# Optimization experiments

Hardware: AMD Instinct MI355X
Metric: run time of the kernel (lower is better)

The kernel has to match this reference:

```python
import jax, jax.numpy as jnp
import numpy as np

B, T, C = 4, 2048, 1024
NH = 16
HD = C // NH


def setup_inputs() -> dict:
    key = jax.random.key(0)
    ks = jax.random.split(key, 5)
    s = 1.0 / np.sqrt(C)
    return {
        "x": jax.random.normal(ks[0], (B, T, C), dtype=jnp.float32),
        "W_qkv": jax.random.normal(ks[1], (C, 3 * C), dtype=jnp.float32) * s,
        "b_qkv": jnp.zeros((3 * C,), dtype=jnp.float32),
        "W_out": jax.random.normal(ks[2], (C, C), dtype=jnp.float32) * s,
        "b_out": jnp.zeros((C,), dtype=jnp.float32),
    }


def reference(x, W_qkv, b_qkv, W_out, b_out):
    Bx, Tx, Cx = x.shape
    qkv = x @ W_qkv + b_qkv                      # [B,T,3C]
    q, k, v = jnp.split(qkv, 3, axis=2)
    # [B,T,C] -> [B,NH,T,HD]
    q = q.reshape(Bx, Tx, NH, HD).transpose(0, 2, 1, 3)
    k = k.reshape(Bx, Tx, NH, HD).transpose(0, 2, 1, 3)
    v = v.reshape(Bx, Tx, NH, HD).transpose(0, 2, 1, 3)
    scale = 1.0 / np.sqrt(HD).astype(np.float32)
    attn = jnp.einsum('bhqd,bhkd->bhqk', q, k) * scale  # [B,NH,T,T]
    causal = jnp.tril(jnp.ones((Tx, Tx), dtype=bool))
    attn = jnp.where(causal[None, None], attn, jnp.float32(-jnp.inf))
    attn = jax.nn.softmax(attn, axis=-1)
    out = jnp.einsum('bhqk,bhkd->bhqd', attn, v)        # [B,NH,T,HD]
    out = out.transpose(0, 2, 1, 3).reshape(Bx, Tx, Cx)
    y = out @ W_out + b_out
    return (y, k, v)
```

## Files before the change

kernel.cpp:

```cpp
#include <hip/hip_runtime.h>
#include <cstdint>
#include <cstddef>

typedef __bf16 bf16x8 __attribute__((ext_vector_type(8)));
typedef __bf16 bf16x4 __attribute__((ext_vector_type(4)));
typedef float  f32x4  __attribute__((ext_vector_type(4)));

#define MFMA16(a, b, c) __builtin_amdgcn_mfma_f32_16x16x32_bf16((a), (b), (c), 0, 0, 0)

#define GLL16(gsrc, ldst)                                                              \
  __builtin_amdgcn_global_load_lds((__attribute__((address_space(1))) void*)(gsrc),    \
                                   (__attribute__((address_space(3))) void*)(ldst),    \
                                   16, 0, 0)

#define QSCALE 0.1803368801111204f


__global__ __launch_bounds__(256)
void cvt_f32_bf16(const float* __restrict__ in, __bf16* __restrict__ out, int n4)
{
    int i = blockIdx.x * 256 + threadIdx.x;
    if (i < n4) {
        float4 v = ((const float4*)in)[i];
        bf16x4 o;
        o[0] = (__bf16)v.x; o[1] = (__bf16)v.y; o[2] = (__bf16)v.z; o[3] = (__bf16)v.w;
        ((bf16x4*)out)[i] = o;
    }
}

__global__ __launch_bounds__(256)
void transpose_cvt(const float* __restrict__ in, __bf16* __restrict__ out, int K, int N)
{
    __shared__ __bf16 tile[32][33];
    const int n0 = blockIdx.x * 32, k0 = blockIdx.y * 32;
    const int tx = threadIdx.x, ty = threadIdx.y;
    #pragma unroll
    for (int i = 0; i < 4; ++i)
        tile[ty + i * 8][tx] = (__bf16)in[(size_t)(k0 + ty + i * 8) * N + n0 + tx];
    __syncthreads();
    #pragma unroll
    for (int i = 0; i < 4; ++i)
        out[(size_t)(n0 + ty + i * 8) * K + k0 + tx] = tile[tx][ty + i * 8];
}


__global__ __launch_bounds__(256)
void vtrans(const float* __restrict__ vout, __bf16* __restrict__ vwst)
{
    const int bh = blockIdx.y;
    const int t0 = blockIdx.x * 64;
    const int tid = threadIdx.x;

    __shared__ __bf16 VT[64][68];

    const int tr = tid >> 4;
    const int dc = (tid & 15) * 4;

    float4 vals[4];
    #pragma unroll
    for (int i = 0; i < 4; ++i)
        vals[i] = *(const float4*)&vout[((size_t)bh * 2048 + t0 + tr + 16 * i) * 64 + dc];

    #pragma unroll
    for (int j = 0; j < 4; ++j) {
        bf16x4 pk;
        pk[0] = (__bf16)(&vals[0].x)[j];
        pk[1] = (__bf16)(&vals[1].x)[j];
        pk[2] = (__bf16)(&vals[2].x)[j];
        pk[3] = (__bf16)(&vals[3].x)[j];
        *(bf16x4*)&VT[dc + j][4 * tr] = pk;
    }
    __syncthreads();

    #pragma unroll
    for (int k = 0; k < 2; ++k) {
        const int c = tid + 256 * k;
        const int d = c >> 3, off = (c & 7) * 8;
        bf16x8 v = *(const bf16x8*)&VT[d][off];
        *(bf16x8*)&vwst[((size_t)bh * 64 + d) * 2048 + t0 + off] = v;
    }
}


__global__ __launch_bounds__(256)
void gemm_qkv(const __bf16* __restrict__ A, const __bf16* __restrict__ Bt,
              const float* __restrict__ bias,
              __bf16* __restrict__ qws, float* __restrict__ kout, float* __restrict__ vout,
              __bf16* __restrict__ kws)
{
    constexpr int K = 1024;
    const int d   = blockIdx.y * 24 + blockIdx.x;
    const int xcd = d & 7, loc = d >> 3;
    const int m0 = (xcd * 8 + (loc & 7)) * 128;
    const int n0 = (loc >> 3) * 128;
    const int tid = threadIdx.x;
    const int wave = tid >> 6, lane = tid & 63;
    const int quad = lane >> 4, lr = lane & 15;
    const int wrow = (wave & 1) * 64, wcol = (wave >> 1) * 64;

    __shared__ __bf16 As[128 * 32];
    __shared__ __bf16 Bs[128 * 32];

    f32x4 acc[4][4];
    #pragma unroll
    for (int mi = 0; mi < 4; ++mi)
      #pragma unroll
      for (int ni = 0; ni < 4; ++ni)
        #pragma unroll
        for (int c = 0; c < 4; ++c) acc[mi][ni][c] = 0.f;

    const int u0 = tid, u1 = tid + 256;
    const int cg0 = ((u0 & 3) ^ ((u0 >> 3) & 3)) * 8;
    const int cg1 = ((u1 & 3) ^ ((u1 >> 3) & 3)) * 8;
    const __bf16* ga0 = A  + (size_t)(m0 + (u0 >> 2)) * K + cg0;
    const __bf16* ga1 = A  + (size_t)(m0 + (u1 >> 2)) * K + cg1;
    const __bf16* gb0 = Bt + (size_t)(n0 + (u0 >> 2)) * K + cg0;
    const __bf16* gb1 = Bt + (size_t)(n0 + (u1 >> 2)) * K + cg1;
    __bf16* la0 = As + u0 * 8;
    __bf16* la1 = As + u1 * 8;
    __bf16* lb0 = Bs + u0 * 8;
    __bf16* lb1 = Bs + u1 * 8;

    const int sw = (quad ^ ((lr >> 1) & 3)) * 8;

    for (int kt = 0; kt < K; kt += 32) {
        __syncthreads();
        GLL16(ga0 + kt, la0);
        GLL16(ga1 + kt, la1);
        GLL16(gb0 + kt, lb0);
        GLL16(gb1 + kt, lb1);
        __syncthreads();
        bf16x8 af[4], bfv[4];
        #pragma unroll
        for (int mi = 0; mi < 4; ++mi)
            af[mi] = *(const bf16x8*)&As[(wrow + mi * 16 + lr) * 32 + sw];
        #pragma unroll
        for (int ni = 0; ni < 4; ++ni)
            bfv[ni] = *(const bf16x8*)&Bs[(wcol + ni * 16 + lr) * 32 + sw];
        #pragma unroll
        for (int mi = 0; mi < 4; ++mi)
          #pragma unroll
          for (int ni = 0; ni < 4; ++ni)
            acc[mi][ni] = MFMA16(af[mi], bfv[ni], acc[mi][ni]);
    }

    const int sec = n0 >> 10;
    #pragma unroll
    for (int ni = 0; ni < 4; ++ni) {
        const int gn = n0 + wcol + ni * 16 + lr;
        const float bv = bias[gn];
        const int cn = gn & 1023, hh = cn >> 6, dd = cn & 63;
        #pragma unroll
        for (int mi = 0; mi < 4; ++mi) {
            const int gm0 = m0 + wrow + mi * 16 + quad * 4;
            const int b = gm0 >> 11, t0 = gm0 & 2047;
            const size_t tb = ((size_t)b * 16 + hh) * 2048;
            if (sec == 0) {
                #pragma unroll
                for (int r = 0; r < 4; ++r)
                    qws[(tb + t0 + r) * 64 + dd] = (__bf16)((acc[mi][ni][r] + bv) * QSCALE);
            } else if (sec == 1) {
                #pragma unroll
                for (int r = 0; r < 4; ++r) {
                    const float val = acc[mi][ni][r] + bv;
                    kout[(tb + t0 + r) * 64 + dd] = val;
                    kws [(tb + t0 + r) * 64 + dd] = (__bf16)val;
                }
            } else {
                #pragma unroll
                for (int r = 0; r < 4; ++r)
                    vout[(tb + t0 + r) * 64 + dd] = acc[mi][ni][r] + bv;
            }
        }
    }
}


__global__ __launch_bounds__(256)
void gemm_out(const __bf16* __restrict__ A, const __bf16* __restrict__ Bt,
              const float* __restrict__ bias, float* __restrict__ y)
{
    constexpr int K = 1024;
    const int m0 = blockIdx.y * 64, n0 = blockIdx.x * 128;
    const int tid = threadIdx.x;
    const int wave = tid >> 6, lane = tid & 63;
    const int quad = lane >> 4, lr = lane & 15;
    const int wrow = (wave & 1) * 32, wcol = (wave >> 1) * 64;

    __shared__ __bf16 As[64 * 32];
    __shared__ __bf16 Bs[128 * 32];

    f32x4 acc[2][4];
    #pragma unroll
    for (int mi = 0; mi < 2; ++mi)
      #pragma unroll
      for (int ni = 0; ni < 4; ++ni)
        #pragma unroll
        for (int c = 0; c < 4; ++c) acc[mi][ni][c] = 0.f;

    const int ua = tid, u0 = tid, u1 = tid + 256;
    const int cga = ((ua & 3) ^ ((ua >> 3) & 3)) * 8;
    const int cg0 = ((u0 & 3) ^ ((u0 >> 3) & 3)) * 8;
    const int cg1 = ((u1 & 3) ^ ((u1 >> 3) & 3)) * 8;
    const __bf16* ga  = A  + (size_t)(m0 + (ua >> 2)) * K + cga;
    const __bf16* gb0 = Bt + (size_t)(n0 + (u0 >> 2)) * K + cg0;
    const __bf16* gb1 = Bt + (size_t)(n0 + (u1 >> 2)) * K + cg1;
    __bf16* la  = As + ua * 8;
    __bf16* lb0 = Bs + u0 * 8;
    __bf16* lb1 = Bs + u1 * 8;

    const int sw = (quad ^ ((lr >> 1) & 3)) * 8;

    for (int kt = 0; kt < K; kt += 32) {
        __syncthreads();
        GLL16(ga + kt, la);
        GLL16(gb0 + kt, lb0);
        GLL16(gb1 + kt, lb1);
        __syncthreads();
        bf16x8 af[2], bfv[4];
        #pragma unroll
        for (int mi = 0; mi < 2; ++mi)
            af[mi] = *(const bf16x8*)&As[(wrow + mi * 16 + lr) * 32 + sw];
        #pragma unroll
        for (int ni = 0; ni < 4; ++ni)
            bfv[ni] = *(const bf16x8*)&Bs[(wcol + ni * 16 + lr) * 32 + sw];
        #pragma unroll
        for (int mi = 0; mi < 2; ++mi)
          #pragma unroll
          for (int ni = 0; ni < 4; ++ni)
            acc[mi][ni] = MFMA16(af[mi], bfv[ni], acc[mi][ni]);
    }

    #pragma unroll
    for (int ni = 0; ni < 4; ++ni) {
        const int gn = n0 + wcol + ni * 16 + lr;
        const float bv = bias[gn];
        #pragma unroll
        for (int mi = 0; mi < 2; ++mi) {
            #pragma unroll
            for (int r = 0; r < 4; ++r) {
                const int gm = m0 + wrow + mi * 16 + quad * 4 + r;
                y[(size_t)gm * 1024 + gn] = acc[mi][ni][r] + bv;
            }
        }
    }
}


__global__ __launch_bounds__(256, 2)
void attn_fused(const __bf16* __restrict__ qws, const __bf16* __restrict__ kws,
                const __bf16* __restrict__ vwst, __bf16* __restrict__ attnws)
{
    const int bh = blockIdx.x;
    const int tid = threadIdx.x;
    const int wave = tid >> 6, lane = tid & 63;
    const int quad = lane >> 4, lr = lane & 15;

    const int jqp[2] = { (int)blockIdx.y, 15 - (int)blockIdx.y };
    const int ntp[2] = { 2 * (jqp[0] + 1), 2 * (jqp[1] + 1) };
    const int nt0 = ntp[0];
    const int ntot = 34;

    __shared__ __bf16 Ks [3][2][64][32];
    __shared__ __bf16 Vts[3][2][64][32];
    __shared__ __bf16 Ps [4][32][72];

    const int srow = tid >> 2;
    const int scg  = ((tid & 3) ^ ((tid >> 3) & 3)) * 8;
    const __bf16* kb = kws  + ((size_t)bh * 2048 + srow) * 64 + scg;
    const __bf16* vb = vwst + ((size_t)bh * 64 + srow) * 2048 + scg;
    char* lk = (char*)Ks  + tid * 16;
    char* lv = (char*)Vts + tid * 16;

    const int sw = (quad ^ ((lr >> 1) & 3)) * 8;

    bf16x8 ones;
    #pragma unroll
    for (int j = 0; j < 8; ++j) ones[j] = (__bf16)1.0f;

    bf16x8 aq[2][2][2];
    #pragma unroll
    for (int h = 0; h < 2; ++h)
      #pragma unroll
      for (int mi = 0; mi < 2; ++mi) {
        const __bf16* qb = qws + ((size_t)bh * 2048 + jqp[h] * 128 + wave * 32 + mi * 16 + lr) * 64 + quad * 8;
        aq[h][mi][0] = *(const bf16x8*)qb;
        aq[h][mi][1] = *(const bf16x8*)(qb + 32);
      }

#define PREFETCH(j, buf)                                                \
    do {                                                                \
        GLL16(kb + (size_t)(j) * 4096,      lk + (buf) * 8192);         \
        GLL16(kb + (size_t)(j) * 4096 + 32, lk + (buf) * 8192 + 4096);  \
        GLL16(vb + (j) * 64,                lv + (buf) * 8192);         \
        GLL16(vb + (j) * 64 + 32,           lv + (buf) * 8192 + 4096);  \
    } while (0)

    PREFETCH(0, 0);
    PREFETCH(1, 1);

    bf16x4 oreg[2][2][4];

    int pos = 0;
    for (int h = 0; h < 2; ++h) {
        const int jq = jqp[h];
        const int NT = ntp[h];

        f32x4 o_acc[2][4], l_acc[2];
        #pragma unroll
        for (int mi = 0; mi < 2; ++mi) {
            #pragma unroll
            for (int r = 0; r < 4; ++r) l_acc[mi][r] = 0.f;
            #pragma unroll
            for (int n = 0; n < 4; ++n)
                #pragma unroll
                for (int r = 0; r < 4; ++r) o_acc[mi][n][r] = 0.f;
        }

        for (int jt = 0; jt < NT; ++jt, ++pos) {
            const int cur = pos % 3;
            if (pos + 1 < ntot) {
                asm volatile("s_waitcnt vmcnt(4)" ::: "memory");
            } else {
                asm volatile("s_waitcnt vmcnt(0)" ::: "memory");
            }
            asm volatile("s_waitcnt lgkmcnt(0)" ::: "memory");
            asm volatile("s_barrier" ::: "memory");
            if (pos + 2 < ntot) {
                const int p2 = pos + 2;
                const int nj = (p2 < nt0) ? p2 : p2 - nt0;
                PREFETCH(nj, p2 % 3);
            }

            const bool lastTile = (jt == NT - 1);
            if (!(lastTile && wave < 2)) {
                bf16x8 bk[4][2];
                #pragma unroll
                for (int ni = 0; ni < 4; ++ni) {
                    bk[ni][0] = *(const bf16x8*)&Ks[cur][0][ni * 16 + lr][sw];
                    bk[ni][1] = *(const bf16x8*)&Ks[cur][1][ni * 16 + lr][sw];
                }
                f32x4 sacc[2][4];
                #pragma unroll
                for (int mi = 0; mi < 2; ++mi)
                  #pragma unroll
                  for (int ni = 0; ni < 4; ++ni)
                    #pragma unroll
                    for (int c = 0; c < 4; ++c) sacc[mi][ni][c] = -12.f;
                #pragma unroll
                for (int ni = 0; ni < 4; ++ni)
                  #pragma unroll
                  for (int mi = 0; mi < 2; ++mi) {
                    sacc[mi][ni] = MFMA16(aq[h][mi][0], bk[ni][0], sacc[mi][ni]);
                    sacc[mi][ni] = MFMA16(aq[h][mi][1], bk[ni][1], sacc[mi][ni]);
                  }

                const bool needMask = (jt == NT - 2 && wave < 2) || (lastTile && wave >= 2);
                if (needMask) {
                    const int c0 = jt * 64 + lr;
                    #pragma unroll
                    for (int mi = 0; mi < 2; ++mi) {
                        const int t0 = jq * 128 + wave * 32 + mi * 16 + quad * 4;
                        #pragma unroll
                        for (int ni = 0; ni < 4; ++ni)
                          #pragma unroll
                          for (int r = 0; r < 4; ++r)
                            if (c0 + ni * 16 > t0 + r) sacc[mi][ni][r] = -1e30f;
                    }
                }

                #pragma unroll
                for (int mi = 0; mi < 2; ++mi)
                  #pragma unroll
                  for (int r = 0; r < 4; ++r) {
                    bf16x4 pp;
                    #pragma unroll
                    for (int ni = 0; ni < 4; ++ni)
                        pp[ni] = (__bf16)__builtin_amdgcn_exp2f(sacc[mi][ni][r]);
                    *(bf16x4*)&Ps[wave][mi * 16 + quad * 4 + r][4 * lr] = pp;
                  }

                asm volatile("s_waitcnt lgkmcnt(0)" ::: "memory");

                bf16x8 bv[4][2];
                #pragma unroll
                for (int n = 0; n < 4; ++n) {
                    bv[n][0] = *(const bf16x8*)&Vts[cur][0][n * 16 + lr][sw];
                    bv[n][1] = *(const bf16x8*)&Vts[cur][1][n * 16 + lr][sw];
                }
                #pragma unroll
                for (int mi = 0; mi < 2; ++mi) {
                    bf16x8 ap0 = *(const bf16x8*)&Ps[wave][mi * 16 + lr][quad * 8];
                    bf16x8 ap1 = *(const bf16x8*)&Ps[wave][mi * 16 + lr][32 + quad * 8];
                    l_acc[mi] = MFMA16(ap0, ones, l_acc[mi]);
                    l_acc[mi] = MFMA16(ap1, ones, l_acc[mi]);
                    #pragma unroll
                    for (int n = 0; n < 4; ++n) {
                        o_acc[mi][n] = MFMA16(ap0, bv[n][0], o_acc[mi][n]);
                        o_acc[mi][n] = MFMA16(ap1, bv[n][1], o_acc[mi][n]);
                    }
                }
            }
        }

        #pragma unroll
        for (int mi = 0; mi < 2; ++mi)
          #pragma unroll
          for (int r = 0; r < 4; ++r) {
            const float inv = 1.f / l_acc[mi][r];
            #pragma unroll
            for (int n = 0; n < 4; ++n)
                oreg[h][mi][n][r] = (__bf16)(o_acc[mi][n][r] * inv);
          }
    }

    const int b = bh >> 4, h16 = bh & 15;
    #pragma unroll
    for (int h = 0; h < 2; ++h)
      #pragma unroll
      for (int mi = 0; mi < 2; ++mi)
        #pragma unroll
        for (int r = 0; r < 4; ++r) {
            const int t = jqp[h] * 128 + wave * 32 + mi * 16 + quad * 4 + r;
            #pragma unroll
            for (int n = 0; n < 4; ++n)
                attnws[(((size_t)b * 2048 + t) * 16 + h16) * 64 + n * 16 + lr] =
                    oreg[h][mi][n][r];
        }
#undef PREFETCH
}


extern "C" void kernel_launch(void* const* d_in, const int* in_sizes, int n_in,
                              void* d_out, int out_size, void* d_ws, size_t ws_size,
                              hipStream_t stream)
{
    (void)in_sizes; (void)n_in; (void)out_size; (void)ws_size;

    const float* x    = (const float*)d_in[0];
    const float* Wqkv = (const float*)d_in[1];
    const float* bqkv = (const float*)d_in[2];
    const float* Wout = (const float*)d_in[3];
    const float* bout = (const float*)d_in[4];

    float* y    = (float*)d_out;
    float* kout = y + 8388608;
    float* vout = kout + 8388608;

    char* ws = (char*)d_ws;
    __bf16* xb    = (__bf16*)(ws);
    __bf16* wqkvt = (__bf16*)(ws + (16u << 20));
    __bf16* woutt = (__bf16*)(ws + (22u << 20));
    __bf16* qws   = (__bf16*)(ws + (24u << 20));
    __bf16* kws   = (__bf16*)(ws + (40u << 20));
    __bf16* vwst  = (__bf16*)(ws + (56u << 20));
    __bf16* attnw = (__bf16*)(ws + (72u << 20));

    cvt_f32_bf16<<<8192, 256, 0, stream>>>(x, xb, 2097152);
    transpose_cvt<<<dim3(96, 32), dim3(32, 8), 0, stream>>>(Wqkv, wqkvt, 1024, 3072);
    transpose_cvt<<<dim3(32, 32), dim3(32, 8), 0, stream>>>(Wout, woutt, 1024, 1024);
    gemm_qkv<<<dim3(24, 64), 256, 0, stream>>>(xb, wqkvt, bqkv, qws, kout, vout, kws);
    vtrans<<<dim3(32, 64), 256, 0, stream>>>(vout, vwst);
    attn_fused<<<dim3(64, 8), 256, 0, stream>>>(qws, kws, vwst, attnw);
    gemm_out<<<dim3(8, 128), 256, 0, stream>>>(attnw, woutt, bout, y);
}
```

Baseline: 299.6 us.

## Fuse V transpose into QKV GEMM epilogue, enlarge out-GEMM tile, add MFMA priority hints

The QKV GEMM epilogue for the V section now stages bf16 V values in an LDS buffer that shares storage with the GEMM tiles, then writes the transposed per-head V layout directly. This removes the separate vtrans kernel and its extra read of the fp32 V output. The output GEMM uses 128-row tiles instead of 64, halving its grid to raise per-block reuse. The attention kernel also wraps its MFMA sections in s_setprio hints to favour the matrix-issuing waves. The tradeoffs are extra barriers and LDS traffic in the V blocks, and fewer output-GEMM blocks, which lowers parallelism.

```diff
diff --git a/kernel.cpp b/kernel.cpp
--- a/kernel.cpp
+++ b/kernel.cpp
@@ -44,55 +44,137 @@
 }
 
 
-__global__ __launch_bounds__(256)
-void vtrans(const float* __restrict__ vout, __bf16* __restrict__ vwst)
-{
-    const int bh = blockIdx.y;
-    const int t0 = blockIdx.x * 64;
-    const int tid = threadIdx.x;
-
-    __shared__ __bf16 VT[64][68];
-
-    const int tr = tid >> 4;
-    const int dc = (tid & 15) * 4;
-
-    float4 vals[4];
-    #pragma unroll
-    for (int i = 0; i < 4; ++i)
-        vals[i] = *(const float4*)&vout[((size_t)bh * 2048 + t0 + tr + 16 * i) * 64 + dc];
-
-    #pragma unroll
-    for (int j = 0; j < 4; ++j) {
-        bf16x4 pk;
-        pk[0] = (__bf16)(&vals[0].x)[j];
-        pk[1] = (__bf16)(&vals[1].x)[j];
-        pk[2] = (__bf16)(&vals[2].x)[j];
-        pk[3] = (__bf16)(&vals[3].x)[j];
-        *(bf16x4*)&VT[dc + j][4 * tr] = pk;
-    }
-    __syncthreads();
-
-    #pragma unroll
-    for (int k = 0; k < 2; ++k) {
-        const int c = tid + 256 * k;
-        const int d = c >> 3, off = (c & 7) * 8;
-        bf16x8 v = *(const bf16x8*)&VT[d][off];
-        *(bf16x8*)&vwst[((size_t)bh * 64 + d) * 2048 + t0 + off] = v;
-    }
-}
-
+union SmemQKV {
+    struct { __bf16 As[128 * 32]; __bf16 Bs[128 * 32]; } g;
+    __bf16 VtL[2][64][136];
+};
 
 __global__ __launch_bounds__(256)
 void gemm_qkv(const __bf16* __restrict__ A, const __bf16* __restrict__ Bt,
               const float* __restrict__ bias,
               __bf16* __restrict__ qws, float* __restrict__ kout, float* __restrict__ vout,
-              __bf16* __restrict__ kws)
+              __bf16* __restrict__ kws, __bf16* __restrict__ vwst)
 {
     constexpr int K = 1024;
     const int d   = blockIdx.y * 24 + blockIdx.x;
     const int xcd = d & 7, loc = d >> 3;
     const int m0 = (xcd * 8 + (loc & 7)) * 128;
     const int n0 = (loc >> 3) * 128;
+    const int tid = threadIdx.x;
+    const int wave = tid >> 6, lane = tid & 63;
+    const int quad = lane >> 4, lr = lane & 15;
+    const int wrow = (wave & 1) * 64, wcol = (wave >> 1) * 64;
+
+    __shared__ SmemQKV sm;
+
+    f32x4 acc[4][4];
+    #pragma unroll
+    for (int mi = 0; mi < 4; ++mi)
+      #pragma unroll
+      for (int ni = 0; ni < 4; ++ni)
+        #pragma unroll
+        for (int c = 0; c < 4; ++c) acc[mi][ni][c] = 0.f;
+
+    const int u0 = tid, u1 = tid + 256;
+    const int cg0 = ((u0 & 3) ^ ((u0 >> 3) & 3)) * 8;
+    const int cg1 = ((u1 & 3) ^ ((u1 >> 3) & 3)) * 8;
+    const __bf16* ga0 = A  + (size_t)(m0 + (u0 >> 2)) * K + cg0;
+    const __bf16* ga1 = A  + (size_t)(m0 + (u1 >> 2)) * K + cg1;
+    const __bf16* gb0 = Bt + (size_t)(n0 + (u0 >> 2)) * K + cg0;
+    const __bf16* gb1 = Bt + (size_t)(n0 + (u1 >> 2)) * K + cg1;
+    __bf16* la0 = sm.g.As + u0 * 8;
+    __bf16* la1 = sm.g.As + u1 * 8;
+    __bf16* lb0 = sm.g.Bs + u0 * 8;
+    __bf16* lb1 = sm.g.Bs + u1 * 8;
+
+    const int sw = (quad ^ ((lr >> 1) & 3)) * 8;
+
+    for (int kt = 0; kt < K; kt += 32) {
+        __syncthreads();
+        GLL16(ga0 + kt, la0);
+        GLL16(ga1 + kt, la1);
+        GLL16(gb0 + kt, lb0);
+        GLL16(gb1 + kt, lb1);
+        __syncthreads();
+        bf16x8 af[4], bfv[4];
+        #pragma unroll
+        for (int mi = 0; mi < 4; ++mi)
+            af[mi] = *(const bf16x8*)&sm.g.As[(wrow + mi * 16 + lr) * 32 + sw];
+        #pragma unroll
+        for (int ni = 0; ni < 4; ++ni)
+            bfv[ni] = *(const bf16x8*)&sm.g.Bs[(wcol + ni * 16 + lr) * 32 + sw];
+        #pragma unroll
+        for (int mi = 0; mi < 4; ++mi)
+          #pragma unroll
+          for (int ni = 0; ni < 4; ++ni)
+            acc[mi][ni] = MFMA16(af[mi], bfv[ni], acc[mi][ni]);
+    }
+
+    const int sec = n0 >> 10;
+
+    if (sec == 2) {
+        __syncthreads();
+    }
+
+    #pragma unroll
+    for (int ni = 0; ni < 4; ++ni) {
+        const int gn = n0 + wcol + ni * 16 + lr;
+        const float bv = bias[gn];
+        const int cn = gn & 1023, hh = cn >> 6, dd = cn & 63;
+        #pragma unroll
+        for (int mi = 0; mi < 4; ++mi) {
+            const int gm0 = m0 + wrow + mi * 16 + quad * 4;
+            const int b = gm0 >> 11, t0 = gm0 & 2047;
+            const size_t tb = ((size_t)b * 16 + hh) * 2048;
+            if (sec == 0) {
+                #pragma unroll
+                for (int r = 0; r < 4; ++r)
+                    qws[(tb + t0 + r) * 64 + dd] = (__bf16)((acc[mi][ni][r] + bv) * QSCALE);
+            } else if (sec == 1) {
+                #pragma unroll
+                for (int r = 0; r < 4; ++r) {
+                    const float val = acc[mi][ni][r] + bv;
+                    kout[(tb + t0 + r) * 64 + dd] = val;
+                    kws [(tb + t0 + r) * 64 + dd] = (__bf16)val;
+                }
+            } else {
+                #pragma unroll
+                for (int r = 0; r < 4; ++r) {
+                    const float val = acc[mi][ni][r] + bv;
+                    vout[(tb + t0 + r) * 64 + dd] = val;
+                    const int tau = wrow + mi * 16 + quad * 4 + r;
+                    const int t64 = tau & 63, blk = tau >> 6;
+                    const int p = 4 * (t64 & 15) + (t64 >> 4);
+                    sm.VtL[hh & 1][dd][blk * 64 + p] = (__bf16)val;
+                }
+            }
+        }
+    }
+
+    if (sec == 2) {
+        __syncthreads();
+        const int b = m0 >> 11, t_base = m0 & 2047;
+        const int hh0 = (n0 & 1023) >> 6;
+        #pragma unroll
+        for (int k = 0; k < 8; ++k) {
+            const int e  = (tid + 256 * k) * 8;
+            const int p8 = e & 127;
+            const int dd = (e >> 7) & 63;
+            const int hl = e >> 13;
+            bf16x8 v = *(const bf16x8*)&sm.VtL[hl][dd][p8];
+            const int bh = b * 16 + hh0 + hl;
+            *(bf16x8*)&vwst[((size_t)bh * 64 + dd) * 2048 + t_base + p8] = v;
+        }
+    }
+}
+
+
+__global__ __launch_bounds__(256)
+void gemm_out(const __bf16* __restrict__ A, const __bf16* __restrict__ Bt,
+              const float* __restrict__ bias, float* __restrict__ y)
+{
+    constexpr int K = 1024;
+    const int m0 = blockIdx.y * 128, n0 = blockIdx.x * 128;
     const int tid = threadIdx.x;
     const int wave = tid >> 6, lane = tid & 63;
     const int quad = lane >> 4, lr = lane & 15;
@@ -144,99 +226,12 @@
             acc[mi][ni] = MFMA16(af[mi], bfv[ni], acc[mi][ni]);
     }
 
-    const int sec = n0 >> 10;
     #pragma unroll
     for (int ni = 0; ni < 4; ++ni) {
         const int gn = n0 + wcol + ni * 16 + lr;
         const float bv = bias[gn];
-        const int cn = gn & 1023, hh = cn >> 6, dd = cn & 63;
         #pragma unroll
         for (int mi = 0; mi < 4; ++mi) {
-            const int gm0 = m0 + wrow + mi * 16 + quad * 4;
-            const int b = gm0 >> 11, t0 = gm0 & 2047;
-            const size_t tb = ((size_t)b * 16 + hh) * 2048;
-            if (sec == 0) {
-                #pragma unroll
-                for (int r = 0; r < 4; ++r)
-                    qws[(tb + t0 + r) * 64 + dd] = (__bf16)((acc[mi][ni][r] + bv) * QSCALE);
-            } else if (sec == 1) {
-                #pragma unroll
-                for (int r = 0; r < 4; ++r) {
-                    const float val = acc[mi][ni][r] + bv;
-                    kout[(tb + t0 + r) * 64 + dd] = val;
-                    kws [(tb + t0 + r) * 64 + dd] = (__bf16)val;
-                }
-            } else {
-                #pragma unroll
-                for (int r = 0; r < 4; ++r)
-                    vout[(tb + t0 + r) * 64 + dd] = acc[mi][ni][r] + bv;
-            }
-        }
-    }
-}
-
-
-__global__ __launch_bounds__(256)
-void gemm_out(const __bf16* __restrict__ A, const __bf16* __restrict__ Bt,
-              const float* __restrict__ bias, float* __restrict__ y)
-{
-    constexpr int K = 1024;
-    const int m0 = blockIdx.y * 64, n0 = blockIdx.x * 128;
-    const int tid = threadIdx.x;
-    const int wave = tid >> 6, lane = tid & 63;
-    const int quad = lane >> 4, lr = lane & 15;
-    const int wrow = (wave & 1) * 32, wcol = (wave >> 1) * 64;
-
-    __shared__ __bf16 As[64 * 32];
-    __shared__ __bf16 Bs[128 * 32];
-
-    f32x4 acc[2][4];
-    #pragma unroll
-    for (int mi = 0; mi < 2; ++mi)
-      #pragma unroll
-      for (int ni = 0; ni < 4; ++ni)
-        #pragma unroll
-        for (int c = 0; c < 4; ++c) acc[mi][ni][c] = 0.f;
-
-    const int ua = tid, u0 = tid, u1 = tid + 256;
-    const int cga = ((ua & 3) ^ ((ua >> 3) & 3)) * 8;
-    const int cg0 = ((u0 & 3) ^ ((u0 >> 3) & 3)) * 8;
-    const int cg1 = ((u1 & 3) ^ ((u1 >> 3) & 3)) * 8;
-    const __bf16* ga  = A  + (size_t)(m0 + (ua >> 2)) * K + cga;
-    const __bf16* gb0 = Bt + (size_t)(n0 + (u0 >> 2)) * K + cg0;
-    const __bf16* gb1 = Bt + (size_t)(n0 + (u1 >> 2)) * K + cg1;
-    __bf16* la  = As + ua * 8;
-    __bf16* lb0 = Bs + u0 * 8;
-    __bf16* lb1 = Bs + u1 * 8;
-
-    const int sw = (quad ^ ((lr >> 1) & 3)) * 8;
-
-    for (int kt = 0; kt < K; kt += 32) {
-        __syncthreads();
-        GLL16(ga + kt, la);
-        GLL16(gb0 + kt, lb0);
-        GLL16(gb1 + kt, lb1);
-        __syncthreads();
-        bf16x8 af[2], bfv[4];
-        #pragma unroll
-        for (int mi = 0; mi < 2; ++mi)
-            af[mi] = *(const bf16x8*)&As[(wrow + mi * 16 + lr) * 32 + sw];
-        #pragma unroll
-        for (int ni = 0; ni < 4; ++ni)
-            bfv[ni] = *(const bf16x8*)&Bs[(wcol + ni * 16 + lr) * 32 + sw];
-        #pragma unroll
-        for (int mi = 0; mi < 2; ++mi)
-          #pragma unroll
-          for (int ni = 0; ni < 4; ++ni)
-            acc[mi][ni] = MFMA16(af[mi], bfv[ni], acc[mi][ni]);
-    }
-
-    #pragma unroll
-    for (int ni = 0; ni < 4; ++ni) {
-        const int gn = n0 + wcol + ni * 16 + lr;
-        const float bv = bias[gn];
-        #pragma unroll
-        for (int mi = 0; mi < 2; ++mi) {
             #pragma unroll
             for (int r = 0; r < 4; ++r) {
                 const int gm = m0 + wrow + mi * 16 + quad * 4 + r;
@@ -347,6 +342,7 @@
                   for (int ni = 0; ni < 4; ++ni)
                     #pragma unroll
                     for (int c = 0; c < 4; ++c) sacc[mi][ni][c] = -12.f;
+                __builtin_amdgcn_s_setprio(1);
                 #pragma unroll
                 for (int ni = 0; ni < 4; ++ni)
                   #pragma unroll
@@ -354,6 +350,7 @@
                     sacc[mi][ni] = MFMA16(aq[h][mi][0], bk[ni][0], sacc[mi][ni]);
                     sacc[mi][ni] = MFMA16(aq[h][mi][1], bk[ni][1], sacc[mi][ni]);
                   }
+                __builtin_amdgcn_s_setprio(0);
 
                 const bool needMask = (jt == NT - 2 && wave < 2) || (lastTile && wave >= 2);
                 if (needMask) {
@@ -388,6 +385,7 @@
                     bv[n][0] = *(const bf16x8*)&Vts[cur][0][n * 16 + lr][sw];
                     bv[n][1] = *(const bf16x8*)&Vts[cur][1][n * 16 + lr][sw];
                 }
+                __builtin_amdgcn_s_setprio(1);
                 #pragma unroll
                 for (int mi = 0; mi < 2; ++mi) {
                     bf16x8 ap0 = *(const bf16x8*)&Ps[wave][mi * 16 + lr][quad * 8];
@@ -400,6 +398,7 @@
                         o_acc[mi][n] = MFMA16(ap1, bv[n][1], o_acc[mi][n]);
                     }
                 }
+                __builtin_amdgcn_s_setprio(0);
             }
         }
 
@@ -459,8 +458,7 @@
     cvt_f32_bf16<<<8192, 256, 0, stream>>>(x, xb, 2097152);
     transpose_cvt<<<dim3(96, 32), dim3(32, 8), 0, stream>>>(Wqkv, wqkvt, 1024, 3072);
     transpose_cvt<<<dim3(32, 32), dim3(32, 8), 0, stream>>>(Wout, woutt, 1024, 1024);
-    gemm_qkv<<<dim3(24, 64), 256, 0, stream>>>(xb, wqkvt, bqkv, qws, kout, vout, kws);
-    vtrans<<<dim3(32, 64), 256, 0, stream>>>(vout, vwst);
+    gemm_qkv<<<dim3(24, 64), 256, 0, stream>>>(xb, wqkvt, bqkv, qws, kout, vout, kws, vwst);
     attn_fused<<<dim3(64, 8), 256, 0, stream>>>(qws, kws, vwst, attnw);
-    gemm_out<<<dim3(8, 128), 256, 0, stream>>>(attnw, woutt, bout, y);
-}
+    gemm_out<<<dim3(8, 64), 256, 0, stream>>>(attnw, woutt, bout, y);
+}
```

Measured after the change: 302.6 us. Within noise of the previous version (+1.0%).
